# Optimization experiments

Hardware: AMD Instinct MI355X
Metric: run time of the kernel (lower is better)

## Reference

```python
import jax, jax.numpy as jnp
import numpy as np

B, L, D, H = 65536, 20, 4, 1024
T = 61  # output_length; 60 RK4 steps


def setup_inputs() -> dict:
    key = jax.random.key(0)
    ks = jax.random.split(key, 16)
    # small positive states so the quadratic SEIR dynamics stay finite over 60 steps
    xx = jax.random.uniform(ks[0], (B, L, D), dtype=jnp.float32) * 0.1
    dims = [L * D] + [H] * 6 + [3]
    inp = {"xx": xx}
    for i in range(7):
        scale = 1.0 / np.sqrt(dims[i])
        W = jax.random.normal(ks[1 + 2 * i], (dims[i], dims[i + 1]), dtype=jnp.float32) * scale
        if i == 6:
            W = W * 1e-3  # keep beta/gamma/sigma small -> stable integration
        inp[f"W{i}"] = W
        inp[f"b{i}"] = jnp.zeros((dims[i + 1],), jnp.float32)
    inp["output_length"] = T
    return inp


def reference(xx, W0, b0, W1, b1, W2, b2, W3, b3, W4, b4, W5, b5, W6, b6, output_length):
    h = xx.reshape(xx.shape[0], -1)  # (B, L*D)
    for W, b in ((W0, b0), (W1, b1), (W2, b2), (W3, b3), (W4, b4), (W5, b5)):
        h = jax.nn.leaky_relu(h @ W + b, negative_slope=0.01)
    out = h @ W6 + b6  # (B, 3)
    beta, gamma, sigma = out[:, 0:1], out[:, 1:2], out[:, 2:3]  # each (B,1)

    initial = xx[:, 0]  # (B, 4) = S,E,I,R at t0
    S0, E0, I0, R0 = (initial[:, i:i + 1] for i in range(4))
    # self.step = 1 in the torch module, so dt is folded in as 1.0

    def derivs(S, E, I):
        SI = beta * S * I
        return -SI, SI - sigma * E, sigma * E - gamma * I, gamma * I

    def body(carry, _):
        S, E, I, R = carry
        k1S, k1E, k1I, k1R = derivs(S, E, I)
        k2S, k2E, k2I, k2R = derivs(S + 0.5 * k1S, E + 0.5 * k1E, I + 0.5 * k1I)
        k3S, k3E, k3I, k3R = derivs(S + 0.5 * k2S, E + 0.5 * k2E, I + 0.5 * k2I)
        k4S, k4E, k4I, k4R = derivs(S + k3S, E + k3E, I + k3I)
        upd = lambda f, k1, k2, k3, k4: f + (k1 + 2 * k2 + 2 * k3 + k4) / 6.0
        new = (upd(S, k1S, k2S, k3S, k4S),
               upd(E, k1E, k2E, k3E, k4E),
               upd(I, k1I, k2I, k3I, k4I),
               upd(R, k1R, k2R, k3R, k4R))
        return new, jnp.concatenate(new, axis=1)  # (B,4) per step

    _, ys = jax.lax.scan(body, (S0, E0, I0, R0), None, length=output_length - 1)
    y0 = jnp.concatenate([S0, E0, I0, R0], axis=1)  # (B,4)
    y = jnp.concatenate([y0[None], ys], axis=0)     # (T,B,4)
    return jnp.transpose(y, (1, 0, 2))              # (B,T,4) in S,E,I,R order
```

## Files before the change

### kernel.cpp

```cpp
#include <hip/hip_runtime.h>
#include <stdint.h>

typedef short s16x8 __attribute__((ext_vector_type(8)));
typedef __bf16 bf16x8 __attribute__((ext_vector_type(8)));
typedef float f32x4 __attribute__((ext_vector_type(4)));

typedef const __attribute__((address_space(1))) void* gas_ptr;
typedef __attribute__((address_space(3))) void* las_ptr;

__device__ __forceinline__ unsigned short f2bf(float f) {
  unsigned u = __builtin_bit_cast(unsigned, f);
  u += 0x7FFFu + ((u >> 16) & 1u);
  return (unsigned short)(u >> 16);
}
__device__ __forceinline__ float bf2f(unsigned short h) {
  return __builtin_bit_cast(float, (unsigned)h << 16);
}
__device__ __forceinline__ void async16(const void* g, void* l) {
  __builtin_amdgcn_global_load_lds((gas_ptr)g, (las_ptr)l, 16, 0, 0);
}

__global__ void prep_x0(const float* __restrict__ xx, unsigned short* __restrict__ X0,
                        int rowOffset, int rows) {
  int idx = blockIdx.x * blockDim.x + threadIdx.x;
  if (idx >= rows * 128) return;
  int r = idx >> 7, c = idx & 127;
  float v = (c < 80) ? xx[(size_t)(rowOffset + r) * 80 + c] : 0.f;
  X0[(size_t)r * 128 + c] = f2bf(v);
}

__global__ void transpose_cast(const float* __restrict__ W, unsigned short* __restrict__ WT,
                               int K, int N, int KP) {
  __shared__ float tile[32][33];
  int n0 = blockIdx.x * 32, k0 = blockIdx.y * 32;
  int tx = threadIdx.x, ty = threadIdx.y;
  #pragma unroll
  for (int j = 0; j < 32; j += 8) {
    int k = k0 + ty + j;
    tile[ty + j][tx] = (k < K) ? W[(size_t)k * N + n0 + tx] : 0.f;
  }
  __syncthreads();
  #pragma unroll
  for (int j = 0; j < 32; j += 8) {
    WT[(size_t)(n0 + ty + j) * KP + k0 + tx] = f2bf(tile[tx][ty + j]);
  }
}

#define BM 128
#define BN 128
#define BK 64

__global__ void gemm_mlp(const unsigned short* __restrict__ A,
                         const unsigned short* __restrict__ BT,
                         const float* __restrict__ bias,
                         unsigned short* __restrict__ C,
                         int M, int N, int K, int leaky) {
  __shared__ unsigned short As[BM * BK];
  __shared__ unsigned short Bs[BN * BK];

  const int tid  = threadIdx.x;
  const int wid  = tid >> 6;
  const int lane = tid & 63;
  const int wr = (wid >> 1) * 64;
  const int wc = (wid & 1) * 64;
  const int bn = blockIdx.x * BN;
  const int bm = blockIdx.y * BM;

  const int srow = lane >> 3;
  const int scol = (lane & 7) * 8;

  f32x4 acc[4][4] = {};

  const unsigned short* aTile = A  + (size_t)bm * K;
  const unsigned short* bTile = BT + (size_t)bn * K;

  for (int k0 = 0; k0 < K; k0 += BK) {
    #pragma unroll
    for (int j = 0; j < 4; ++j) {
      const int rg = wid + j * 4;
      async16(aTile + (size_t)(rg * 8 + srow) * K + k0 + scol, &As[rg * 8 * BK]);
      async16(bTile + (size_t)(rg * 8 + srow) * K + k0 + scol, &Bs[rg * 8 * BK]);
    }
    __syncthreads();

    const int fr = lane & 15;
    const int kq = (lane >> 4) * 8;
    #pragma unroll
    for (int ks = 0; ks < BK; ks += 32) {
      const int kk = ks + kq;
      bf16x8 af[4], bv[4];
      #pragma unroll
      for (int m = 0; m < 4; ++m)
        af[m] = __builtin_bit_cast(bf16x8, *(const s16x8*)&As[(wr + m * 16 + fr) * BK + kk]);
      #pragma unroll
      for (int n = 0; n < 4; ++n)
        bv[n] = __builtin_bit_cast(bf16x8, *(const s16x8*)&Bs[(wc + n * 16 + fr) * BK + kk]);
      #pragma unroll
      for (int m = 0; m < 4; ++m)
        #pragma unroll
        for (int n = 0; n < 4; ++n)
          acc[m][n] = __builtin_amdgcn_mfma_f32_16x16x32_bf16(af[m], bv[n], acc[m][n], 0, 0, 0);
    }
    __syncthreads();
  }

  const int fcol = lane & 15;
  const int frow = (lane >> 4) * 4;
  #pragma unroll
  for (int m = 0; m < 4; ++m) {
    #pragma unroll
    for (int n = 0; n < 4; ++n) {
      const int col = bn + wc + n * 16 + fcol;
      const float bb = bias[col];
      #pragma unroll
      for (int r = 0; r < 4; ++r) {
        const int row = bm + wr + m * 16 + frow + r;
        float v = acc[m][n][r] + bb;
        if (leaky) v = (v > 0.f) ? v : 0.01f * v;
        C[(size_t)row * N + col] = f2bf(v);
      }
    }
  }
}


__device__ __forceinline__ void stage_half(const char* srcRow0, size_t ldb,
                                           char* ldsHalf, int w, int rsub, int usw) {
  #pragma unroll
  for (int l = 0; l < 2; ++l) {
    const char* src = srcRow0 + (size_t)((l * 8 + w) * 8 + rsub) * ldb + usw;
    async16(src, ldsHalf + (l * 8 + w) * 1024);
  }
}

#define MFMA16 __builtin_amdgcn_mfma_f32_16x16x32_bf16
#define EPAD 72
#define EBYTES (64 * EPAD * 2)

__global__ __launch_bounds__(512, 2)
void gemm8(const unsigned short* __restrict__ A,
           const unsigned short* __restrict__ BT,
           const float* __restrict__ bias,
           unsigned short* __restrict__ C,
           int M, int N, int K) {
  extern __shared__ char smem[];
  char* smA = smem;
  char* smB = smem + 65536;
  const unsigned short* sA = (const unsigned short*)smA;
  const unsigned short* sB = (const unsigned short*)smB;
  const int NTk = K >> 6;

  const int tid  = threadIdx.x;
  const int w    = tid >> 6;
  const int lane = tid & 63;

  const int nwg = gridDim.x;
  const int bid = blockIdx.x;
  const int q = nwg >> 3, r = nwg & 7;
  const int xcd = bid & 7, idx = bid >> 3;
  const int wg = (xcd < r ? xcd * (q + 1) : r * (q + 1) + (xcd - r) * q) + idx;
  const int nNT = N >> 8;
  const int mtile = wg / nNT, ntile = wg % nNT;
  const int bm = mtile << 8, bn = ntile << 8;

  const int wr = (w >> 2) << 7;
  const int wc = (w & 3) << 6;
  const int fr = lane & 15;
  const int e0 = lane >> 4;
  const int sw = lane & 7;
  const int rsub = lane >> 3;
  const int usw  = ((sw ^ rsub) << 4);
  const int col0 = (((e0)     ^ sw) << 3);
  const int col1 = (((e0 + 4) ^ sw) << 3);

  const size_t ldb = (size_t)K * 2;
  const char* Ab = (const char*)A  + (size_t)bm * ldb;
  const char* Bb = (const char*)BT + (size_t)bn * ldb;

  f32x4 acc[8][4] = {};

#define RDA(c_, row_, col_) __builtin_bit_cast(bf16x8, *(const s16x8*)&sA[(c_) * 16384 + (row_) * 64 + (col_)])
#define RDB(c_, row_, col_) __builtin_bit_cast(bf16x8, *(const s16x8*)&sB[(c_) * 16384 + (row_) * 64 + (col_)])

  stage_half(Bb,                    ldb, smB,                  w, rsub, usw);
  stage_half(Bb + 128 * ldb,        ldb, smB + 16384,          w, rsub, usw);
  stage_half(Ab,                    ldb, smA,                  w, rsub, usw);
  stage_half(Ab + 128 * ldb,        ldb, smA + 16384,          w, rsub, usw);
  stage_half(Bb + 128,              ldb, smB + 32768,          w, rsub, usw);
  stage_half(Bb + 128 * ldb + 128,  ldb, smB + 32768 + 16384,  w, rsub, usw);
  asm volatile("s_waitcnt vmcnt(4)" ::: "memory");
  __builtin_amdgcn_s_barrier();

  for (int kt = 0; kt < NTk; ++kt) {
    const int c = kt & 1;
    bf16x8 aF[4][2], bF[4][2];

    #pragma unroll
    for (int m = 0; m < 4; ++m) {
      const int row = wr + m * 16 + fr;
      aF[m][0] = RDA(c, row, col0);
      aF[m][1] = RDA(c, row, col1);
    }
    #pragma unroll
    for (int n = 0; n < 2; ++n) {
      const int row = wc + n * 16 + fr;
      bF[n][0] = RDB(c, row, col0);
      bF[n][1] = RDB(c, row, col1);
    }
    if (kt + 1 < NTk)
      stage_half(Ab + (size_t)(kt + 1) * 128, ldb, smA + (c ^ 1) * 32768, w, rsub, usw);
    __builtin_amdgcn_s_barrier();
    __builtin_amdgcn_s_setprio(1);
    #pragma unroll
    for (int m = 0; m < 4; ++m)
      #pragma unroll
      for (int n = 0; n < 2; ++n) {
        acc[m][n] = MFMA16(aF[m][0], bF[n][0], acc[m][n], 0, 0, 0);
        acc[m][n] = MFMA16(aF[m][1], bF[n][1], acc[m][n], 0, 0, 0);
      }
    __builtin_amdgcn_s_setprio(0);
    __builtin_amdgcn_s_barrier();

    #pragma unroll
    for (int n = 2; n < 4; ++n) {
      const int row = wc + n * 16 + fr;
      bF[n][0] = RDB(c, row, col0);
      bF[n][1] = RDB(c, row, col1);
    }
    if (kt + 1 < NTk)
      stage_half(Ab + 128 * ldb + (size_t)(kt + 1) * 128, ldb,
                 smA + (c ^ 1) * 32768 + 16384, w, rsub, usw);
    __builtin_amdgcn_s_barrier();
    __builtin_amdgcn_s_setprio(1);
    #pragma unroll
    for (int m = 0; m < 4; ++m)
      #pragma unroll
      for (int n = 2; n < 4; ++n) {
        acc[m][n] = MFMA16(aF[m][0], bF[n][0], acc[m][n], 0, 0, 0);
        acc[m][n] = MFMA16(aF[m][1], bF[n][1], acc[m][n], 0, 0, 0);
      }
    __builtin_amdgcn_s_setprio(0);
    __builtin_amdgcn_s_barrier();

    #pragma unroll
    for (int m = 0; m < 4; ++m) {
      const int row = wr + (m + 4) * 16 + fr;
      aF[m][0] = RDA(c, row, col0);
      aF[m][1] = RDA(c, row, col1);
    }
    if (kt + 2 < NTk)
      stage_half(Bb + (size_t)(kt + 2) * 128, ldb, smB + c * 32768, w, rsub, usw);
    __builtin_amdgcn_s_barrier();
    __builtin_amdgcn_s_setprio(1);
    #pragma unroll
    for (int m = 0; m < 4; ++m)
      #pragma unroll
      for (int n = 0; n < 2; ++n) {
        acc[m + 4][n] = MFMA16(aF[m][0], bF[n][0], acc[m + 4][n], 0, 0, 0);
        acc[m + 4][n] = MFMA16(aF[m][1], bF[n][1], acc[m + 4][n], 0, 0, 0);
      }
    __builtin_amdgcn_s_setprio(0);
    __builtin_amdgcn_s_barrier();

    if (kt + 2 < NTk)
      stage_half(Bb + 128 * ldb + (size_t)(kt + 2) * 128, ldb,
                 smB + c * 32768 + 16384, w, rsub, usw);
    __builtin_amdgcn_s_barrier();
    __builtin_amdgcn_s_setprio(1);
    #pragma unroll
    for (int m = 0; m < 4; ++m)
      #pragma unroll
      for (int n = 2; n < 4; ++n) {
        acc[m + 4][n] = MFMA16(aF[m][0], bF[n][0], acc[m + 4][n], 0, 0, 0);
        acc[m + 4][n] = MFMA16(aF[m][1], bF[n][1], acc[m + 4][n], 0, 0, 0);
      }
    __builtin_amdgcn_s_setprio(0);
    if (kt + 2 < NTk) asm volatile("s_waitcnt vmcnt(4)" ::: "memory");
    else              asm volatile("s_waitcnt vmcnt(0)" ::: "memory");
    __builtin_amdgcn_s_barrier();
  }

#undef RDA
#undef RDB

  unsigned short* eb = (unsigned short*)(smem + w * EBYTES);
  const int fcol = lane & 15;
  float bbv[4];
  #pragma unroll
  for (int n = 0; n < 4; ++n) bbv[n] = bias[bn + wc + n * 16 + fcol];
  const int r8 = lane >> 3, c8 = (lane & 7) * 8;
  #pragma unroll
  for (int mh = 0; mh < 2; ++mh) {
    #pragma unroll
    for (int mm = 0; mm < 4; ++mm)
      #pragma unroll
      for (int n = 0; n < 4; ++n)
        #pragma unroll
        for (int rr = 0; rr < 4; ++rr) {
          const int row64 = mm * 16 + e0 * 4 + rr;
          float v = acc[mh * 4 + mm][n][rr] + bbv[n];
          v = (v > 0.f) ? v : 0.01f * v;
          eb[row64 * EPAD + n * 16 + fcol] = f2bf(v);
        }
    asm volatile("" ::: "memory");
    #pragma unroll
    for (int rg = 0; rg < 8; ++rg) {
      const int row64 = rg * 8 + r8;
      s16x8 vv = *(const s16x8*)&eb[row64 * EPAD + c8];
      const int rl = bm + wr + mh * 64 + row64;
      *(s16x8*)&C[(size_t)rl * N + bn + wc + c8] = vv;
    }
    asm volatile("" ::: "memory");
  }
}

__global__ void head_gemv(const unsigned short* __restrict__ H,
                          const float* __restrict__ W6,
                          const float* __restrict__ b6,
                          float* __restrict__ bgs,
                          int rows) {
  const int w = (blockIdx.x * blockDim.x + threadIdx.x) >> 6;
  const int lane = threadIdx.x & 63;
  if (w >= rows) return;

  const unsigned short* h = H + (size_t)w * 1024 + lane * 16;
  float s0 = 0.f, s1 = 0.f, s2 = 0.f;
  #pragma unroll
  for (int i = 0; i < 16; i += 8) {
    s16x8 v = *(const s16x8*)(h + i);
    #pragma unroll
    for (int j = 0; j < 8; ++j) {
      const float hv = bf2f((unsigned short)v[j]);
      const int e = lane * 16 + i + j;
      s0 = fmaf(hv, W6[e * 3 + 0], s0);
      s1 = fmaf(hv, W6[e * 3 + 1], s1);
      s2 = fmaf(hv, W6[e * 3 + 2], s2);
    }
  }
  #pragma unroll
  for (int off = 1; off < 64; off <<= 1) {
    s0 += __shfl_xor(s0, off);
    s1 += __shfl_xor(s1, off);
    s2 += __shfl_xor(s2, off);
  }
  if (lane == 0) {
    float4 v = make_float4(s0 + b6[0], s1 + b6[1], s2 + b6[2], 0.f);
    *(float4*)(bgs + (size_t)w * 4) = v;
  }
}

__global__ void rk4_traj(const float* __restrict__ bgs,
                         const float* __restrict__ xx,
                         float* __restrict__ out,
                         int rowOffset, int rows, int T) {
  const int r = blockIdx.x * blockDim.x + threadIdx.x;
  if (r >= rows) return;
  const size_t grow = (size_t)rowOffset + r;

  const float4 bg = *(const float4*)(bgs + (size_t)r * 4);
  const float beta = bg.x, gamma = bg.y, sigma = bg.z;

  const float4 iv = *(const float4*)(xx + grow * 80);
  float S = iv.x, E = iv.y, I = iv.z, R = iv.w;
  float* o = out + grow * (size_t)T * 4;
  *(float4*)o = iv;

#define DERIVS(S_, E_, I_, dS, dE, dI, dR)      \
  {                                             \
    float SI = beta * (S_) * (I_);              \
    float sE = sigma * (E_);                    \
    float gI = gamma * (I_);                    \
    dS = -SI; dE = SI - sE; dI = sE - gI; dR = gI; \
  }

  for (int t = 1; t < T; ++t) {
    float k1S, k1E, k1I, k1R; DERIVS(S, E, I, k1S, k1E, k1I, k1R);
    float k2S, k2E, k2I, k2R; DERIVS(S + 0.5f * k1S, E + 0.5f * k1E, I + 0.5f * k1I, k2S, k2E, k2I, k2R);
    float k3S, k3E, k3I, k3R; DERIVS(S + 0.5f * k2S, E + 0.5f * k2E, I + 0.5f * k2I, k3S, k3E, k3I, k3R);
    float k4S, k4E, k4I, k4R; DERIVS(S + k3S, E + k3E, I + k3I, k4S, k4E, k4I, k4R);
    S += (k1S + 2.f * k2S + 2.f * k3S + k4S) * (1.f / 6.f);
    E += (k1E + 2.f * k2E + 2.f * k3E + k4E) * (1.f / 6.f);
    I += (k1I + 2.f * k2I + 2.f * k3I + k4I) * (1.f / 6.f);
    R += (k1R + 2.f * k2R + 2.f * k3R + k4R) * (1.f / 6.f);
    *(float4*)(o + (size_t)t * 4) = make_float4(S, E, I, R);
  }
#undef DERIVS
}

extern "C" void kernel_launch(void* const* d_in, const int* in_sizes, int n_in,
                              void* d_out, int out_size, void* d_ws, size_t ws_size,
                              hipStream_t stream) {
  const float* xx = (const float*)d_in[0];
  const float* W[7];
  const float* bb[7];
  for (int i = 0; i < 7; ++i) {
    W[i]  = (const float*)d_in[1 + 2 * i];
    bb[i] = (const float*)d_in[2 + 2 * i];
  }
  const int B = in_sizes[0] / 80;
  const int T = out_size / (B * 4);
  float* out = (float*)d_out;

  hipFuncSetAttribute((const void*)gemm8,
                      hipFuncAttributeMaxDynamicSharedMemorySize, 131072);

  uint8_t* ws = (uint8_t*)d_ws;
  size_t off = 0;
  auto alloc = [&](size_t bytes) -> uint8_t* {
    uint8_t* p = ws + off;
    off += (bytes + 255) & ~(size_t)255;
    return p;
  };

  unsigned short* WTl[6];
  WTl[0] = (unsigned short*)alloc((size_t)1024 * 128 * 2);
  for (int i = 1; i < 6; ++i) WTl[i] = (unsigned short*)alloc((size_t)1024 * 1024 * 2);

  const size_t weightBytes = off;
  const size_t avail = ws_size > weightBytes ? ws_size - weightBytes : 0;
  int Bc = (int)(avail / 4368);
  Bc = (Bc / 256) * 256;
  if (Bc > B) Bc = B;
  if (Bc < 256) Bc = 256;

  unsigned short* X0   = (unsigned short*)alloc((size_t)Bc * 128 * 2);
  unsigned short* buf0 = (unsigned short*)alloc((size_t)Bc * 1024 * 2);
  unsigned short* buf1 = (unsigned short*)alloc((size_t)Bc * 1024 * 2);
  float* bgs           = (float*)alloc((size_t)Bc * 4 * 4);

  {
    dim3 blk(32, 8);
    transpose_cast<<<dim3(32, 4), blk, 0, stream>>>(W[0], WTl[0], 80, 1024, 128);
    for (int i = 1; i < 6; ++i)
      transpose_cast<<<dim3(32, 32), blk, 0, stream>>>(W[i], WTl[i], 1024, 1024, 1024);
  }

  for (int r0 = 0; r0 < B; r0 += Bc) {
    const int rows = (B - r0 < Bc) ? (B - r0) : Bc;

    {
      const int n = rows * 128;
      prep_x0<<<(n + 255) / 256, 256, 0, stream>>>(xx, X0, r0, rows);
    }

    gemm_mlp<<<dim3(8, rows / 128), 256, 0, stream>>>(X0, WTl[0], bb[0], buf0,
                                                      rows, 1024, 128, 1);

    const int nwg = (rows / 256) * 4;
    gemm8<<<nwg, 512, 131072, stream>>>(buf0, WTl[1], bb[1], buf1, rows, 1024, 1024);
    gemm8<<<nwg, 512, 131072, stream>>>(buf1, WTl[2], bb[2], buf0, rows, 1024, 1024);
    gemm8<<<nwg, 512, 131072, stream>>>(buf0, WTl[3], bb[3], buf1, rows, 1024, 1024);
    gemm8<<<nwg, 512, 131072, stream>>>(buf1, WTl[4], bb[4], buf0, rows, 1024, 1024);
    gemm8<<<nwg, 512, 131072, stream>>>(buf0, WTl[5], bb[5], buf1, rows, 1024, 1024);

    head_gemv<<<rows / 4, 256, 0, stream>>>(buf1, W[6], bb[6], bgs, rows);
    rk4_traj<<<(rows + 255) / 256, 256, 0, stream>>>(bgs, xx, out, r0, rows, T);
  }
}
```

Measured before the change: 1.012 ms.

## Fuse head GEMV into last GEMM epilogue and batch weight transposes

The final hidden-layer GEMM is templated so its epilogue applies bias and LeakyReLU, then dots each row tile with W6 in registers. It writes per-N-tile partial sums of the three parameters instead of storing the bf16 activation. The RK4 kernel reduces the four partials and adds b6, which removes the head_gemv launch and the write and read of a Bc×1024 activation. The six transpose launches are also merged into one 3D-grid kernel. The trade-off is slightly different rounding, since the head now uses fp32 activations rather than bf16, plus a larger partial buffer.

```diff
diff --git a/kernel.cpp b/kernel.cpp
--- a/kernel.cpp
+++ b/kernel.cpp
@@ -29,15 +29,25 @@
   X0[(size_t)r * 128 + c] = f2bf(v);
 }
 
-__global__ void transpose_cast(const float* __restrict__ W, unsigned short* __restrict__ WT,
-                               int K, int N, int KP) {
+struct TP {
+  const float* W[6];
+  unsigned short* WT[6];
+};
+
+__global__ void transpose_all(TP tp) {
+  const int z = blockIdx.z;
+  const int K  = (z == 0) ? 80  : 1024;
+  const int KP = (z == 0) ? 128 : 1024;
+  if (blockIdx.y * 32 >= KP) return;
   __shared__ float tile[32][33];
-  int n0 = blockIdx.x * 32, k0 = blockIdx.y * 32;
-  int tx = threadIdx.x, ty = threadIdx.y;
+  const int n0 = blockIdx.x * 32, k0 = blockIdx.y * 32;
+  const int tx = threadIdx.x, ty = threadIdx.y;
+  const float* W = tp.W[z];
+  unsigned short* WT = tp.WT[z];
   #pragma unroll
   for (int j = 0; j < 32; j += 8) {
     int k = k0 + ty + j;
-    tile[ty + j][tx] = (k < K) ? W[(size_t)k * N + n0 + tx] : 0.f;
+    tile[ty + j][tx] = (k < K) ? W[(size_t)k * 1024 + n0 + tx] : 0.f;
   }
   __syncthreads();
   #pragma unroll
@@ -137,11 +147,14 @@
 #define EPAD 72
 #define EBYTES (64 * EPAD * 2)
 
+template <int HEAD>
 __global__ __launch_bounds__(512, 2)
 void gemm8(const unsigned short* __restrict__ A,
            const unsigned short* __restrict__ BT,
            const float* __restrict__ bias,
            unsigned short* __restrict__ C,
+           const float* __restrict__ W6,
+           float* __restrict__ partial,
            int M, int N, int K) {
   extern __shared__ char smem[];
   char* smA = smem;
@@ -283,73 +296,78 @@
 #undef RDA
 #undef RDB
 
-  unsigned short* eb = (unsigned short*)(smem + w * EBYTES);
   const int fcol = lane & 15;
   float bbv[4];
   #pragma unroll
   for (int n = 0; n < 4; ++n) bbv[n] = bias[bn + wc + n * 16 + fcol];
-  const int r8 = lane >> 3, c8 = (lane & 7) * 8;
-  #pragma unroll
-  for (int mh = 0; mh < 2; ++mh) {
-    #pragma unroll
-    for (int mm = 0; mm < 4; ++mm)
-      #pragma unroll
-      for (int n = 0; n < 4; ++n)
+
+  if constexpr (HEAD) {
+    float w6c[4][3];
+    #pragma unroll
+    for (int n = 0; n < 4; ++n) {
+      const int col = bn + wc + n * 16 + fcol;
+      #pragma unroll
+      for (int j = 0; j < 3; ++j) w6c[n][j] = W6[col * 3 + j];
+    }
+    const int nt = bn >> 8;
+    #pragma unroll
+    for (int mh = 0; mh < 2; ++mh)
+      #pragma unroll
+      for (int mm = 0; mm < 4; ++mm)
         #pragma unroll
         for (int rr = 0; rr < 4; ++rr) {
-          const int row64 = mm * 16 + e0 * 4 + rr;
-          float v = acc[mh * 4 + mm][n][rr] + bbv[n];
-          v = (v > 0.f) ? v : 0.01f * v;
-          eb[row64 * EPAD + n * 16 + fcol] = f2bf(v);
+          float s0 = 0.f, s1 = 0.f, s2 = 0.f;
+          #pragma unroll
+          for (int n = 0; n < 4; ++n) {
+            float v = acc[mh * 4 + mm][n][rr] + bbv[n];
+            v = (v > 0.f) ? v : 0.01f * v;
+            s0 = fmaf(v, w6c[n][0], s0);
+            s1 = fmaf(v, w6c[n][1], s1);
+            s2 = fmaf(v, w6c[n][2], s2);
+          }
+          #pragma unroll
+          for (int off = 1; off < 16; off <<= 1) {
+            s0 += __shfl_xor(s0, off);
+            s1 += __shfl_xor(s1, off);
+            s2 += __shfl_xor(s2, off);
+          }
+          if (fcol == 0) {
+            const int row = bm + wr + mh * 64 + mm * 16 + e0 * 4 + rr;
+            *(float4*)&partial[((size_t)nt * M + row) * 4] =
+                make_float4(s0, s1, s2, 0.f);
+          }
         }
-    asm volatile("" ::: "memory");
-    #pragma unroll
-    for (int rg = 0; rg < 8; ++rg) {
-      const int row64 = rg * 8 + r8;
-      s16x8 vv = *(const s16x8*)&eb[row64 * EPAD + c8];
-      const int rl = bm + wr + mh * 64 + row64;
-      *(s16x8*)&C[(size_t)rl * N + bn + wc + c8] = vv;
-    }
-    asm volatile("" ::: "memory");
-  }
-}
-
-__global__ void head_gemv(const unsigned short* __restrict__ H,
-                          const float* __restrict__ W6,
-                          const float* __restrict__ b6,
-                          float* __restrict__ bgs,
-                          int rows) {
-  const int w = (blockIdx.x * blockDim.x + threadIdx.x) >> 6;
-  const int lane = threadIdx.x & 63;
-  if (w >= rows) return;
-
-  const unsigned short* h = H + (size_t)w * 1024 + lane * 16;
-  float s0 = 0.f, s1 = 0.f, s2 = 0.f;
-  #pragma unroll
-  for (int i = 0; i < 16; i += 8) {
-    s16x8 v = *(const s16x8*)(h + i);
-    #pragma unroll
-    for (int j = 0; j < 8; ++j) {
-      const float hv = bf2f((unsigned short)v[j]);
-      const int e = lane * 16 + i + j;
-      s0 = fmaf(hv, W6[e * 3 + 0], s0);
-      s1 = fmaf(hv, W6[e * 3 + 1], s1);
-      s2 = fmaf(hv, W6[e * 3 + 2], s2);
-    }
-  }
-  #pragma unroll
-  for (int off = 1; off < 64; off <<= 1) {
-    s0 += __shfl_xor(s0, off);
-    s1 += __shfl_xor(s1, off);
-    s2 += __shfl_xor(s2, off);
-  }
-  if (lane == 0) {
-    float4 v = make_float4(s0 + b6[0], s1 + b6[1], s2 + b6[2], 0.f);
-    *(float4*)(bgs + (size_t)w * 4) = v;
-  }
-}
-
-__global__ void rk4_traj(const float* __restrict__ bgs,
+  } else {
+    unsigned short* eb = (unsigned short*)(smem + w * EBYTES);
+    const int r8 = lane >> 3, c8 = (lane & 7) * 8;
+    #pragma unroll
+    for (int mh = 0; mh < 2; ++mh) {
+      #pragma unroll
+      for (int mm = 0; mm < 4; ++mm)
+        #pragma unroll
+        for (int n = 0; n < 4; ++n)
+          #pragma unroll
+          for (int rr = 0; rr < 4; ++rr) {
+            const int row64 = mm * 16 + e0 * 4 + rr;
+            float v = acc[mh * 4 + mm][n][rr] + bbv[n];
+            v = (v > 0.f) ? v : 0.01f * v;
+            eb[row64 * EPAD + n * 16 + fcol] = f2bf(v);
+          }
+      asm volatile("" ::: "memory");
+      #pragma unroll
+      for (int rg = 0; rg < 8; ++rg) {
+        const int row64 = rg * 8 + r8;
+        s16x8 vv = *(const s16x8*)&eb[row64 * EPAD + c8];
+        const int rl = bm + wr + mh * 64 + row64;
+        *(s16x8*)&C[(size_t)rl * N + bn + wc + c8] = vv;
+      }
+      asm volatile("" ::: "memory");
+    }
+  }
+}
+
+__global__ void rk4_traj(const float* __restrict__ partial,
+                         const float* __restrict__ b6,
                          const float* __restrict__ xx,
                          float* __restrict__ out,
                          int rowOffset, int rows, int T) {
@@ -357,8 +375,13 @@
   if (r >= rows) return;
   const size_t grow = (size_t)rowOffset + r;
 
-  const float4 bg = *(const float4*)(bgs + (size_t)r * 4);
-  const float beta = bg.x, gamma = bg.y, sigma = bg.z;
+  float4 p0 = *(const float4*)&partial[((size_t)0 * rows + r) * 4];
+  float4 p1 = *(const float4*)&partial[((size_t)1 * rows + r) * 4];
+  float4 p2 = *(const float4*)&partial[((size_t)2 * rows + r) * 4];
+  float4 p3 = *(const float4*)&partial[((size_t)3 * rows + r) * 4];
+  const float beta  = p0.x + p1.x + p2.x + p3.x + b6[0];
+  const float gamma = p0.y + p1.y + p2.y + p3.y + b6[1];
+  const float sigma = p0.z + p1.z + p2.z + p3.z + b6[2];
 
   const float4 iv = *(const float4*)(xx + grow * 80);
   float S = iv.x, E = iv.y, I = iv.z, R = iv.w;
@@ -401,8 +424,12 @@
   const int T = out_size / (B * 4);
   float* out = (float*)d_out;
 
-  hipFuncSetAttribute((const void*)gemm8,
-                      hipFuncAttributeMaxDynamicSharedMemorySize, 131072);
+  {
+    auto k0 = gemm8<0>;
+    auto k1 = gemm8<1>;
+    hipFuncSetAttribute((const void*)k0, hipFuncAttributeMaxDynamicSharedMemorySize, 131072);
+    hipFuncSetAttribute((const void*)k1, hipFuncAttributeMaxDynamicSharedMemorySize, 131072);
+  }
 
   uint8_t* ws = (uint8_t*)d_ws;
   size_t off = 0;
@@ -418,7 +445,7 @@
 
   const size_t weightBytes = off;
   const size_t avail = ws_size > weightBytes ? ws_size - weightBytes : 0;
-  int Bc = (int)(avail / 4368);
+  int Bc = (int)(avail / 4416);
   Bc = (Bc / 256) * 256;
   if (Bc > B) Bc = B;
   if (Bc < 256) Bc = 256;
@@ -426,13 +453,12 @@
   unsigned short* X0   = (unsigned short*)alloc((size_t)Bc * 128 * 2);
   unsigned short* buf0 = (unsigned short*)alloc((size_t)Bc * 1024 * 2);
   unsigned short* buf1 = (unsigned short*)alloc((size_t)Bc * 1024 * 2);
-  float* bgs           = (float*)alloc((size_t)Bc * 4 * 4);
+  float* partial       = (float*)alloc((size_t)Bc * 4 * 16);
 
   {
-    dim3 blk(32, 8);
-    transpose_cast<<<dim3(32, 4), blk, 0, stream>>>(W[0], WTl[0], 80, 1024, 128);
-    for (int i = 1; i < 6; ++i)
-      transpose_cast<<<dim3(32, 32), blk, 0, stream>>>(W[i], WTl[i], 1024, 1024, 1024);
+    TP tp;
+    for (int i = 0; i < 6; ++i) { tp.W[i] = W[i]; tp.WT[i] = WTl[i]; }
+    transpose_all<<<dim3(32, 32, 6), dim3(32, 8), 0, stream>>>(tp);
   }
 
   for (int r0 = 0; r0 < B; r0 += Bc) {
@@ -447,13 +473,13 @@
                                                       rows, 1024, 128, 1);
 
     const int nwg = (rows / 256) * 4;
-    gemm8<<<nwg, 512, 131072, stream>>>(buf0, WTl[1], bb[1], buf1, rows, 1024, 1024);
-    gemm8<<<nwg, 512, 131072, stream>>>(buf1, WTl[2], bb[2], buf0, rows, 1024, 1024);
-    gemm8<<<nwg, 512, 131072, stream>>>(buf0, WTl[3], bb[3], buf1, rows, 1024, 1024);
-    gemm8<<<nwg, 512, 131072, stream>>>(buf1, WTl[4], bb[4], buf0, rows, 1024, 1024);
-    gemm8<<<nwg, 512, 131072, stream>>>(buf0, WTl[5], bb[5], buf1, rows, 1024, 1024);
-
-    head_gemv<<<rows / 4, 256, 0, stream>>>(buf1, W[6], bb[6], bgs, rows);
-    rk4_traj<<<(rows + 255) / 256, 256, 0, stream>>>(bgs, xx, out, r0, rows, T);
-  }
-}
+    gemm8<0><<<nwg, 512, 131072, stream>>>(buf0, WTl[1], bb[1], buf1, nullptr, nullptr, rows, 1024, 1024);
+    gemm8<0><<<nwg, 512, 131072, stream>>>(buf1, WTl[2], bb[2], buf0, nullptr, nullptr, rows, 1024, 1024);
+    gemm8<0><<<nwg, 512, 131072, stream>>>(buf0, WTl[3], bb[3], buf1, nullptr, nullptr, rows, 1024, 1024);
+    gemm8<0><<<nwg, 512, 131072, stream>>>(buf1, WTl[4], bb[4], buf0, nullptr, nullptr, rows, 1024, 1024);
+
+    gemm8<1><<<nwg, 512, 131072, stream>>>(buf0, WTl[5], bb[5], nullptr, W[6], partial, rows, 1024, 1024);
+
+    rk4_traj<<<(rows + 255) / 256, 256, 0, stream>>>(partial, bb[6], xx, out, r0, rows, T);
+  }
+}
```

After: 959.9 us. -5.1%, faster.
